# Kernel tuning notes

Measured on AMD Instinct MI355X. Metric: run time of the kernel, lower is better.

Reference implementation:

```python
import jax, jax.numpy as jnp
import numpy as np
import math

N_HEADS = 4


def setup_inputs() -> dict:
    key = jax.random.key(0)
    k1, k2, k3 = jax.random.split(key, 3)
    B, C, T = 4096, 256, 64
    q = jax.random.normal(k1, (B, C, 1), dtype=jnp.float32)
    k = jax.random.normal(k2, (B, C, T), dtype=jnp.float32)
    v = jax.random.normal(k3, (B, C, T), dtype=jnp.float32)
    return {"q": q, "k": k, "v": v,
            "use_gumbel_softmax": 1, "is_train": 0, "hard_mode": 0}


def reference(q, k, v, use_gumbel_softmax, is_train, hard_mode):
    bs, width, length = k.shape
    assert k.shape == v.shape
    assert width % N_HEADS == 0
    ch = width // N_HEADS
    scale = 1.0 / math.sqrt(math.sqrt(ch))

    qh = (q * scale).reshape(bs * N_HEADS, ch, -1)   # [BH, ch, 1]
    kh = (k * scale).reshape(bs * N_HEADS, ch, -1)   # [BH, ch, T]
    vh = v.reshape(bs * N_HEADS, ch, -1)             # [BH, ch, T]

    # [BH, 1, T] attention logits; stable softmax in fp32 then cast back
    weight = jnp.einsum('bct,bcs->bts', qh, kh)
    weight = jax.nn.softmax(weight.astype(jnp.float32), axis=-1).astype(weight.dtype)

    if use_gumbel_softmax:
        # eval path (is_train=False): deterministic argmax one-hot selection
        weight_onehot = (weight == jnp.max(weight, axis=-1, keepdims=True)).astype(jnp.float32)
        weight = weight * weight_onehot
        a = jnp.einsum('bts,bcs->bct', weight_onehot, vh)   # [BH, ch, 1]
    else:
        a = jnp.einsum('bts,bcs->bct', weight, vh)

    weight_sum = jnp.sum(weight, axis=2, keepdims=True)     # [BH, 1, 1]
    if N_HEADS > 1:
        weight_sum = weight_sum.reshape(bs, N_HEADS, -1)
        weight_sum = jnp.sum(weight_sum, axis=1, keepdims=True)  # [B, 1, 1]

    return a.reshape(bs, width, -1), weight_sum
```

## Files before the change

### kernel.cpp

```cpp
#include <hip/hip_runtime.h>
#include <cstdint>


typedef __attribute__((address_space(3))) void lds_t;
typedef const __attribute__((address_space(1))) void glb_t;

__global__ __launch_bounds__(256, 4) void qkv_gumbel_attn(
    const float* __restrict__ q,
    const float* __restrict__ k,
    const float* __restrict__ v,
    float* __restrict__ out_a,
    float* __restrict__ out_ws)
{
    constexpr float SCALE = 0.35355339059327373f;
    const int b   = blockIdx.x;
    const int tid = threadIdx.x;
    const int h   = tid >> 6;
    const int l   = tid & 63;
    const int r4  = l >> 4;

    __shared__ float sk[4][2][1024];
    __shared__ float sq[256];
    __shared__ float sws[4];

    sq[tid] = q[(size_t)b * 256 + tid] * SCALE;
    asm volatile("" ::: "memory");

    const float4* __restrict__ k4 =
        reinterpret_cast<const float4*>(k) + (size_t)b * 4096 + (size_t)h * 1024;

#pragma unroll
    for (int i = 0; i < 4; ++i) {
        __builtin_amdgcn_global_load_lds((glb_t*)(k4 + i * 64 + l),
                                         (lds_t*)&sk[h][0][i * 256], 16, 0, 0);
    }

    float a0 = 0.f, a1 = 0.f, a2 = 0.f, a3 = 0.f;
#pragma unroll
    for (int r = 0; r < 4; ++r) {
        if (r < 3) {
#pragma unroll
            for (int i = 0; i < 4; ++i) {
                __builtin_amdgcn_global_load_lds(
                    (glb_t*)(k4 + (r + 1) * 256 + i * 64 + l),
                    (lds_t*)&sk[h][(r + 1) & 1][i * 256], 16, 0, 0);
            }
            asm volatile("s_waitcnt vmcnt(4)" ::: "memory");
        } else {
            asm volatile("s_waitcnt vmcnt(0)" ::: "memory");
        }
        const float* __restrict__ buf = sk[h][r & 1];
#pragma unroll
        for (int i = 0; i < 4; ++i) {
            const float4 kv =
                *reinterpret_cast<const float4*>(&buf[i * 256 + 4 * l]);
            const float qc = sq[h * 64 + r * 16 + 4 * i + r4];
            a0 = fmaf(qc, kv.x * SCALE, a0);
            a1 = fmaf(qc, kv.y * SCALE, a1);
            a2 = fmaf(qc, kv.z * SCALE, a2);
            a3 = fmaf(qc, kv.w * SCALE, a3);
        }
    }

    a0 += __shfl_xor(a0, 16); a0 += __shfl_xor(a0, 32);
    a1 += __shfl_xor(a1, 16); a1 += __shfl_xor(a1, 32);
    a2 += __shfl_xor(a2, 16); a2 += __shfl_xor(a2, 32);
    a3 += __shfl_xor(a3, 16); a3 += __shfl_xor(a3, 32);

    float m = fmaxf(fmaxf(a0, a1), fmaxf(a2, a3));
#pragma unroll
    for (int off = 1; off <= 8; off <<= 1) m = fmaxf(m, __shfl_xor(m, off));

    const float e0 = expf(a0 - m), e1 = expf(a1 - m),
                e2 = expf(a2 - m), e3 = expf(a3 - m);
    float d = e0 + e1 + e2 + e3;
#pragma unroll
    for (int off = 1; off <= 8; off <<= 1) d += __shfl_xor(d, off);

    const float pm = 1.0f / d;

    uint64_t m0 = __ballot(e0 / d == pm) & 0xFFFFull;
    uint64_t m1 = __ballot(e1 / d == pm) & 0xFFFFull;
    uint64_t m2 = __ballot(e2 / d == pm) & 0xFFFFull;
    uint64_t m3 = __ballot(e3 / d == pm) & 0xFFFFull;

    const int cnt = __popcll(m0) + __popcll(m1) + __popcll(m2) + __popcll(m3);

    const float* __restrict__ vrow =
        v + (size_t)b * 16384 + (size_t)(h * 64 + l) * 64;
    float aval = 0.f;
    while (m0) { int s = __ffsll((unsigned long long)m0) - 1; m0 &= m0 - 1; aval += vrow[4 * s + 0]; }
    while (m1) { int s = __ffsll((unsigned long long)m1) - 1; m1 &= m1 - 1; aval += vrow[4 * s + 1]; }
    while (m2) { int s = __ffsll((unsigned long long)m2) - 1; m2 &= m2 - 1; aval += vrow[4 * s + 2]; }
    while (m3) { int s = __ffsll((unsigned long long)m3) - 1; m3 &= m3 - 1; aval += vrow[4 * s + 3]; }

    out_a[(size_t)b * 256 + tid] = aval;

    if (l == 0) sws[h] = pm * (float)cnt;
    __syncthreads();
    if (tid == 0) out_ws[b] = ((sws[0] + sws[1]) + sws[2]) + sws[3];
}

extern "C" void kernel_launch(void* const* d_in, const int* in_sizes, int n_in,
                              void* d_out, int out_size, void* d_ws, size_t ws_size,
                              hipStream_t stream) {
    const float* q = (const float*)d_in[0];
    const float* k = (const float*)d_in[1];
    const float* v = (const float*)d_in[2];
    float* out_a  = (float*)d_out;
    float* out_ws = out_a + (size_t)4096 * 256;
    qkv_gumbel_attn<<<dim3(4096), dim3(256), 0, stream>>>(q, k, v, out_a, out_ws);
}
```

Measured before the change: 77.12 us.

## Process four batches per block with cross-batch K prefetch and deferred V gather

Each block now handles four consecutive batch rows instead of one. The first K chunk and the q vector of the next batch are prefetched into LDS during the current batch's last round. The single-argmax V load is issued asynchronously and its store is deferred into the next iteration, so the V-gather latency overlaps with K streaming. This targets per-block startup latency and the serialized tail of the old kernel, at the cost of 4x fewer blocks (1024), less parallelism, and fragile hand-counted vmcnt waits.

Measured after the change: 79.42 us. 3.0% more time.

```diff
diff --git a/kernel.cpp b/kernel.cpp
--- a/kernel.cpp
+++ b/kernel.cpp
@@ -4,6 +4,10 @@
 
 typedef __attribute__((address_space(3))) void lds_t;
 typedef const __attribute__((address_space(1))) void glb_t;
+
+#define VWAIT(n) asm volatile("s_waitcnt vmcnt(" #n ")" ::: "memory")
+
+constexpr int NB = 4;
 
 __global__ __launch_bounds__(256, 4) void qkv_gumbel_attn(
     const float* __restrict__ q,
@@ -13,92 +17,136 @@
     float* __restrict__ out_ws)
 {
     constexpr float SCALE = 0.35355339059327373f;
-    const int b   = blockIdx.x;
     const int tid = threadIdx.x;
     const int h   = tid >> 6;
     const int l   = tid & 63;
     const int r4  = l >> 4;
+    const int b0  = blockIdx.x * NB;
 
     __shared__ float sk[4][2][1024];
-    __shared__ float sq[256];
-    __shared__ float sws[4];
+    __shared__ float sq[4][2][64];
+    __shared__ float sws[4][NB];
 
-    sq[tid] = q[(size_t)b * 256 + tid] * SCALE;
-    asm volatile("" ::: "memory");
+    const float4* __restrict__ k4 = reinterpret_cast<const float4*>(k);
 
-    const float4* __restrict__ k4 =
-        reinterpret_cast<const float4*>(k) + (size_t)b * 4096 + (size_t)h * 1024;
+#define STAGE_K(b_, r_, buf_)                                                  \
+    do {                                                                       \
+        _Pragma("unroll")                                                      \
+        for (int i_ = 0; i_ < 4; ++i_)                                         \
+            __builtin_amdgcn_global_load_lds(                                  \
+                (glb_t*)(k4 + (size_t)(b_) * 4096 + h * 1024 + (r_) * 256 +    \
+                         i_ * 64 + l),                                         \
+                (lds_t*)&sk[h][buf_][i_ * 256], 16, 0, 0);                     \
+    } while (0)
 
+#define STAGE_Q(b_, par_)                                                      \
+    __builtin_amdgcn_global_load_lds(                                          \
+        (glb_t*)(q + (size_t)(b_) * 256 + h * 64 + l),                         \
+        (lds_t*)&sq[h][par_][0], 4, 0, 0)
+
+    STAGE_Q(b0, 0);
+    STAGE_K(b0, 0, 0);
+    STAGE_Q(b0, 0);
+
+    float gv = 0.f;
+
+    for (int it = 0; it < NB; ++it) {
+        const int b   = b0 + it;
+        const int par = it & 1;
+        const float* __restrict__ qb = sq[h][par];
+
+        float a0 = 0.f, a1 = 0.f, a2 = 0.f, a3 = 0.f;
+
+#define ROUND(r_)                                                              \
+        do {                                                                   \
+            const float* __restrict__ bufp_ = sk[h][(r_) & 1];                 \
+            _Pragma("unroll")                                                  \
+            for (int i_ = 0; i_ < 4; ++i_) {                                   \
+                const float4 kv_ = *reinterpret_cast<const float4*>(           \
+                    &bufp_[i_ * 256 + 4 * l]);                                 \
+                const float qc_ = qb[(r_) * 16 + 4 * i_ + r4] * SCALE;         \
+                a0 = fmaf(qc_, kv_.x * SCALE, a0);                             \
+                a1 = fmaf(qc_, kv_.y * SCALE, a1);                             \
+                a2 = fmaf(qc_, kv_.z * SCALE, a2);                             \
+                a3 = fmaf(qc_, kv_.w * SCALE, a3);                             \
+            }                                                                  \
+        } while (0)
+
+        STAGE_K(b, 1, 1);
+        VWAIT(5);
+        ROUND(0);
+
+        STAGE_K(b, 2, 0);
+        VWAIT(4);
+        if (it > 0) out_a[(size_t)(b - 1) * 256 + tid] = gv;
+        ROUND(1);
+
+        STAGE_K(b, 3, 1);
+        VWAIT(4);
+        ROUND(2);
+
+        const int bn = (b + 1 < 4096) ? (b + 1) : 4095;
+        STAGE_Q(bn, par ^ 1);
+        STAGE_K(bn, 0, 0);
+        VWAIT(5);
+        ROUND(3);
+
+        a0 += __shfl_xor(a0, 16); a0 += __shfl_xor(a0, 32);
+        a1 += __shfl_xor(a1, 16); a1 += __shfl_xor(a1, 32);
+        a2 += __shfl_xor(a2, 16); a2 += __shfl_xor(a2, 32);
+        a3 += __shfl_xor(a3, 16); a3 += __shfl_xor(a3, 32);
+
+        float m = fmaxf(fmaxf(a0, a1), fmaxf(a2, a3));
 #pragma unroll
-    for (int i = 0; i < 4; ++i) {
-        __builtin_amdgcn_global_load_lds((glb_t*)(k4 + i * 64 + l),
-                                         (lds_t*)&sk[h][0][i * 256], 16, 0, 0);
+        for (int off = 1; off <= 8; off <<= 1) m = fmaxf(m, __shfl_xor(m, off));
+
+        const float e0 = expf(a0 - m), e1 = expf(a1 - m),
+                    e2 = expf(a2 - m), e3 = expf(a3 - m);
+        float d = e0 + e1 + e2 + e3;
+#pragma unroll
+        for (int off = 1; off <= 8; off <<= 1) d += __shfl_xor(d, off);
+
+        const float pm = 1.0f / d;
+
+        uint64_t m0 = __ballot(e0 / d == pm) & 0xFFFFull;
+        uint64_t m1 = __ballot(e1 / d == pm) & 0xFFFFull;
+        uint64_t m2 = __ballot(e2 / d == pm) & 0xFFFFull;
+        uint64_t m3 = __ballot(e3 / d == pm) & 0xFFFFull;
+
+        const int cnt = __popcll(m0) + __popcll(m1) + __popcll(m2) + __popcll(m3);
+        if (l == 0) sws[h][it] = pm * (float)cnt;
+
+        const float* __restrict__ vrow =
+            v + (size_t)b * 16384 + (size_t)(h * 64 + l) * 64;
+
+        if (cnt == 1) {
+            const uint64_t mm = m0 | (m1 << 16) | (m2 << 32) | (m3 << 48);
+            const int bit = __ffsll((unsigned long long)mm) - 1;
+            const float* gaddr = vrow + 4 * (bit & 15) + (bit >> 4);
+            asm volatile("global_load_dword %0, %1, off"
+                         : "=v"(gv) : "v"(gaddr) : "memory");
+        } else {
+            VWAIT(0);
+            float av = 0.f;
+            while (m0) { int s = __ffsll((unsigned long long)m0) - 1; m0 &= m0 - 1; av += vrow[4 * s + 0]; }
+            while (m1) { int s = __ffsll((unsigned long long)m1) - 1; m1 &= m1 - 1; av += vrow[4 * s + 1]; }
+            while (m2) { int s = __ffsll((unsigned long long)m2) - 1; m2 &= m2 - 1; av += vrow[4 * s + 2]; }
+            while (m3) { int s = __ffsll((unsigned long long)m3) - 1; m3 &= m3 - 1; av += vrow[4 * s + 3]; }
+            gv = av;
+        }
+#undef ROUND
     }
 
-    float a0 = 0.f, a1 = 0.f, a2 = 0.f, a3 = 0.f;
-#pragma unroll
-    for (int r = 0; r < 4; ++r) {
-        if (r < 3) {
-#pragma unroll
-            for (int i = 0; i < 4; ++i) {
-                __builtin_amdgcn_global_load_lds(
-                    (glb_t*)(k4 + (r + 1) * 256 + i * 64 + l),
-                    (lds_t*)&sk[h][(r + 1) & 1][i * 256], 16, 0, 0);
-            }
-            asm volatile("s_waitcnt vmcnt(4)" ::: "memory");
-        } else {
-            asm volatile("s_waitcnt vmcnt(0)" ::: "memory");
-        }
-        const float* __restrict__ buf = sk[h][r & 1];
-#pragma unroll
-        for (int i = 0; i < 4; ++i) {
-            const float4 kv =
-                *reinterpret_cast<const float4*>(&buf[i * 256 + 4 * l]);
-            const float qc = sq[h * 64 + r * 16 + 4 * i + r4];
-            a0 = fmaf(qc, kv.x * SCALE, a0);
-            a1 = fmaf(qc, kv.y * SCALE, a1);
-            a2 = fmaf(qc, kv.z * SCALE, a2);
-            a3 = fmaf(qc, kv.w * SCALE, a3);
-        }
+    VWAIT(0);
+    out_a[(size_t)(b0 + NB - 1) * 256 + tid] = gv;
+
+    __syncthreads();
+    if (tid < NB) {
+        out_ws[b0 + tid] =
+            ((sws[0][tid] + sws[1][tid]) + sws[2][tid]) + sws[3][tid];
     }
-
-    a0 += __shfl_xor(a0, 16); a0 += __shfl_xor(a0, 32);
-    a1 += __shfl_xor(a1, 16); a1 += __shfl_xor(a1, 32);
-    a2 += __shfl_xor(a2, 16); a2 += __shfl_xor(a2, 32);
-    a3 += __shfl_xor(a3, 16); a3 += __shfl_xor(a3, 32);
-
-    float m = fmaxf(fmaxf(a0, a1), fmaxf(a2, a3));
-#pragma unroll
-    for (int off = 1; off <= 8; off <<= 1) m = fmaxf(m, __shfl_xor(m, off));
-
-    const float e0 = expf(a0 - m), e1 = expf(a1 - m),
-                e2 = expf(a2 - m), e3 = expf(a3 - m);
-    float d = e0 + e1 + e2 + e3;
-#pragma unroll
-    for (int off = 1; off <= 8; off <<= 1) d += __shfl_xor(d, off);
-
-    const float pm = 1.0f / d;
-
-    uint64_t m0 = __ballot(e0 / d == pm) & 0xFFFFull;
-    uint64_t m1 = __ballot(e1 / d == pm) & 0xFFFFull;
-    uint64_t m2 = __ballot(e2 / d == pm) & 0xFFFFull;
-    uint64_t m3 = __ballot(e3 / d == pm) & 0xFFFFull;
-
-    const int cnt = __popcll(m0) + __popcll(m1) + __popcll(m2) + __popcll(m3);
-
-    const float* __restrict__ vrow =
-        v + (size_t)b * 16384 + (size_t)(h * 64 + l) * 64;
-    float aval = 0.f;
-    while (m0) { int s = __ffsll((unsigned long long)m0) - 1; m0 &= m0 - 1; aval += vrow[4 * s + 0]; }
-    while (m1) { int s = __ffsll((unsigned long long)m1) - 1; m1 &= m1 - 1; aval += vrow[4 * s + 1]; }
-    while (m2) { int s = __ffsll((unsigned long long)m2) - 1; m2 &= m2 - 1; aval += vrow[4 * s + 2]; }
-    while (m3) { int s = __ffsll((unsigned long long)m3) - 1; m3 &= m3 - 1; aval += vrow[4 * s + 3]; }
-
-    out_a[(size_t)b * 256 + tid] = aval;
-
-    if (l == 0) sws[h] = pm * (float)cnt;
-    __syncthreads();
-    if (tid == 0) out_ws[b] = ((sws[0] + sws[1]) + sws[2]) + sws[3];
+#undef STAGE_K
+#undef STAGE_Q
 }
 
 extern "C" void kernel_launch(void* const* d_in, const int* in_sizes, int n_in,
@@ -109,5 +157,5 @@
     const float* v = (const float*)d_in[2];
     float* out_a  = (float*)d_out;
     float* out_ws = out_a + (size_t)4096 * 256;
-    qkv_gumbel_attn<<<dim3(4096), dim3(256), 0, stream>>>(q, k, v, out_a, out_ws);
+    qkv_gumbel_attn<<<dim3(1024), dim3(256), 0, stream>>>(q, k, v, out_a, out_ws);
 }
```
